# Optimization experiments

Hardware: AMD Instinct MI355X
Metric: run time of the kernel (lower is better)

## Reference

```python
import jax, jax.numpy as jnp
import numpy as np

NUM_EMBEDDINGS = 1024
EMBEDDING_DIM = 64
COMMITMENT_COST = 0.25


def setup_inputs() -> dict:
    key = jax.random.key(0)
    k1, k2 = jax.random.split(key)
    z = jax.random.normal(k1, (32, EMBEDDING_DIM, 32, 32), dtype=jnp.float32)
    # matches nn.Embedding init: uniform(-1/K, 1/K)
    codebook = jax.random.uniform(
        k2, (NUM_EMBEDDINGS, EMBEDDING_DIM), dtype=jnp.float32,
        minval=-1.0 / NUM_EMBEDDINGS, maxval=1.0 / NUM_EMBEDDINGS)
    return {"z": z, "codebook": codebook}


def reference(z, codebook):
    B, C, H, W = z.shape  # C == embedding_dim
    zp = jnp.transpose(z, (0, 2, 3, 1))          # [B,H,W,C]
    z_flat = zp.reshape(-1, C)                    # [N,C], N=B*H*W
    # squared euclidean distances to every code: [N,K]
    d = (jnp.sum(z_flat ** 2, axis=1, keepdims=True)
         + jnp.sum(codebook ** 2, axis=1)
         - 2.0 * jnp.matmul(z_flat, codebook.T))
    indices = jnp.argmin(d, axis=1)               # [N]
    z_q = codebook[indices].reshape(zp.shape)     # [B,H,W,C]
    e_latent_loss = jnp.mean((jax.lax.stop_gradient(z_q) - zp) ** 2)
    q_latent_loss = jnp.mean((z_q - jax.lax.stop_gradient(zp)) ** 2)
    loss = q_latent_loss + COMMITMENT_COST * e_latent_loss
    # straight-through estimator
    z_q_st = zp + jax.lax.stop_gradient(z_q - zp)
    z_q_out = jnp.transpose(z_q_st, (0, 3, 1, 2))  # back to NCHW
    return z_q_out, loss, indices
```

## Files before the change

kernel.cpp:

```cpp
#include <hip/hip_runtime.h>
#include <float.h>


#define DIM       64
#define N_EMB     1024
#define N_PX      32768
#define LOSS_OFF  2097152
#define IDX_OFF   2097153
#define LOSS_SCALE 5.9604644775390625e-07f

__device__ __forceinline__ float np_sumsq64(const float* a) {
    #pragma clang fp contract(off)
    float r[8];
    #pragma unroll
    for (int j = 0; j < 8; ++j) {
        float s = a[j] * a[j];
        #pragma unroll
        for (int m = 1; m < 8; ++m) {
            float p = a[j + 8 * m] * a[j + 8 * m];
            s = s + p;
        }
        r[j] = s;
    }
    return ((r[0] + r[1]) + (r[2] + r[3])) + ((r[4] + r[5]) + (r[6] + r[7]));
}

__global__ __launch_bounds__(256, 4)
void vq_argmin(const float* __restrict__ z, const float* __restrict__ cb,
               float* __restrict__ ws_val, int* __restrict__ ws_idx,
               float* __restrict__ out) {
    __shared__ float esq[256];
    __shared__ float cand_val[4 * 64];
    __shared__ int   cand_idx[4 * 64];

    const int tid  = threadIdx.x;
    const int lane = tid & 63;
    const int wave = __builtin_amdgcn_readfirstlane(tid >> 6);
    const int g    = blockIdx.x >> 2;
    const int s    = blockIdx.x & 3;
    const int n0   = g * 64;
    const int b    = n0 >> 10;
    const int hw0  = n0 & 1023;
    const size_t zbase = (size_t)b * 65536 + (size_t)hw0;

    {
        #pragma clang fp contract(off)
        const int k = s * 256 + tid;
        const float* row = cb + (size_t)k * DIM;
        float r[8];
        #pragma unroll
        for (int j = 0; j < 8; ++j) {
            float acc = row[j] * row[j];
            #pragma unroll
            for (int m = 1; m < 8; ++m) {
                float p = row[j + 8 * m] * row[j + 8 * m];
                acc = acc + p;
            }
            r[j] = acc;
        }
        esq[tid] = ((r[0] + r[1]) + (r[2] + r[3])) + ((r[4] + r[5]) + (r[6] + r[7]));
    }

    float vz[DIM];
    #pragma unroll
    for (int c = 0; c < DIM; ++c)
        vz[c] = z[zbase + (size_t)c * 1024 + lane];
    const float zz = np_sumsq64(vz);

    __syncthreads();

    float best = FLT_MAX;
    int   bidx = 0;
    const int kb = s * 256 + wave * 64;
    for (int kk = 0; kk < 64; kk += 4) {
        const int k = kb + kk;
        const float* e = cb + (size_t)k * DIM;
        float d0 = 0.f, d1 = 0.f, d2 = 0.f, d3 = 0.f;
        #pragma unroll
        for (int c = 0; c < DIM; ++c) {
            const float v = vz[c];
            d0 = __builtin_fmaf(e[c],       v, d0);
            d1 = __builtin_fmaf(e[64 + c],  v, d1);
            d2 = __builtin_fmaf(e[128 + c], v, d2);
            d3 = __builtin_fmaf(e[192 + c], v, d3);
        }
        const int le = wave * 64 + kk;
        float s0, s1, s2, s3;
        {
            #pragma clang fp contract(off)
            const float p0 = zz + esq[le];
            const float p1 = zz + esq[le + 1];
            const float p2 = zz + esq[le + 2];
            const float p3 = zz + esq[le + 3];
            s0 = p0 - 2.0f * d0;
            s1 = p1 - 2.0f * d1;
            s2 = p2 - 2.0f * d2;
            s3 = p3 - 2.0f * d3;
        }
        if (s0 < best) { best = s0; bidx = k; }
        if (s1 < best) { best = s1; bidx = k + 1; }
        if (s2 < best) { best = s2; bidx = k + 2; }
        if (s3 < best) { best = s3; bidx = k + 3; }
    }
    cand_val[wave * 64 + lane] = best;
    cand_idx[wave * 64 + lane] = bidx;
    __syncthreads();

    if (tid < 64) {
        float bv = cand_val[tid];
        int   bi = cand_idx[tid];
        #pragma unroll
        for (int w = 1; w < 4; ++w) {
            float v = cand_val[w * 64 + tid];
            int   i = cand_idx[w * 64 + tid];
            if (v < bv || (v == bv && i < bi)) { bv = v; bi = i; }
        }
        ws_val[s * N_PX + n0 + tid] = bv;
        ws_idx[s * N_PX + n0 + tid] = bi;
    }
    if (blockIdx.x == 0 && tid == 0) out[LOSS_OFF] = 0.f;
}

__global__ __launch_bounds__(256, 4)
void vq_out(const float* __restrict__ z, const float* __restrict__ cb,
            const float* __restrict__ ws_val, const int* __restrict__ ws_idx,
            float* __restrict__ out) {
    __shared__ int   fidx[64];
    __shared__ float lred[4];

    const int tid  = threadIdx.x;
    const int lane = tid & 63;
    const int wave = tid >> 6;
    const int n0   = blockIdx.x * 64;
    const int b    = n0 >> 10;
    const int hw0  = n0 & 1023;
    const size_t zbase = (size_t)b * 65536 + (size_t)hw0;

    if (tid < 64) {
        float bv = ws_val[n0 + tid];
        int   bi = ws_idx[n0 + tid];
        #pragma unroll
        for (int sl = 1; sl < 4; ++sl) {
            float v = ws_val[sl * N_PX + n0 + tid];
            int   i = ws_idx[sl * N_PX + n0 + tid];
            if (v < bv || (v == bv && i < bi)) { bv = v; bi = i; }
        }
        fidx[tid] = bi;
        out[IDX_OFF + n0 + tid] = (float)bi;
    }
    __syncthreads();

    const int px = tid & 63;
    const int cg = tid >> 6;
    const int mi = fidx[px];
    float lacc = 0.f;
    #pragma unroll
    for (int i = 0; i < 16; ++i) {
        const int c = cg * 16 + i;
        float q  = cb[mi * DIM + c];
        size_t go = zbase + (size_t)c * 1024 + px;
        float zv = z[go];
        float d  = q - zv;
        lacc = __builtin_fmaf(d, d, lacc);
        out[go] = q;
    }
    #pragma unroll
    for (int off = 32; off > 0; off >>= 1)
        lacc += __shfl_down(lacc, off, 64);
    if (lane == 0) lred[wave] = lacc;
    __syncthreads();
    if (tid == 0) {
        float t = (lred[0] + lred[1]) + (lred[2] + lred[3]);
        atomicAdd(&out[LOSS_OFF], t * LOSS_SCALE);
    }
}

extern "C" void kernel_launch(void* const* d_in, const int* in_sizes, int n_in,
                              void* d_out, int out_size, void* d_ws, size_t ws_size,
                              hipStream_t stream) {
    const float* z  = (const float*)d_in[0];
    const float* cb = (const float*)d_in[1];
    float* out = (float*)d_out;
    float* ws_val = (float*)d_ws;
    int*   ws_idx = (int*)((char*)d_ws + 4u * N_PX * sizeof(float));

    vq_argmin<<<2048, 256, 0, stream>>>(z, cb, ws_val, ws_idx, out);
    vq_out<<<512, 256, 0, stream>>>(z, cb, ws_val, ws_idx, out);
}
```

Before: 151.5 us.

## Stage z tile in LDS as float4 and unroll codebook loop by eight

Instead of each thread holding 64 z values in registers, the block stages its 64-pixel z tile in shared memory as float4 and reads it back inside the distance loop. This frees VGPRs, and launch bounds are raised to allow 8 blocks per CU for higher occupancy. The codebook loop now handles 8 codes per iteration to reuse each LDS z read across more FMAs. The trade is extra LDS traffic and latency inside the hot loop in exchange for occupancy and fewer global z loads.

```diff
diff --git a/kernel.cpp b/kernel.cpp
--- a/kernel.cpp
+++ b/kernel.cpp
@@ -9,15 +9,15 @@
 #define IDX_OFF   2097153
 #define LOSS_SCALE 5.9604644775390625e-07f
 
-__device__ __forceinline__ float np_sumsq64(const float* a) {
+__device__ __forceinline__ float np_sumsq64_row(const float* __restrict__ row) {
     #pragma clang fp contract(off)
     float r[8];
     #pragma unroll
     for (int j = 0; j < 8; ++j) {
-        float s = a[j] * a[j];
+        float s = row[j] * row[j];
         #pragma unroll
         for (int m = 1; m < 8; ++m) {
-            float p = a[j + 8 * m] * a[j + 8 * m];
+            float p = row[j + 8 * m] * row[j + 8 * m];
             s = s + p;
         }
         r[j] = s;
@@ -25,13 +25,14 @@
     return ((r[0] + r[1]) + (r[2] + r[3])) + ((r[4] + r[5]) + (r[6] + r[7]));
 }
 
-__global__ __launch_bounds__(256, 4)
+__global__ __launch_bounds__(256, 8)
 void vq_argmin(const float* __restrict__ z, const float* __restrict__ cb,
                float* __restrict__ ws_val, int* __restrict__ ws_idx,
                float* __restrict__ out) {
-    __shared__ float esq[256];
-    __shared__ float cand_val[4 * 64];
-    __shared__ int   cand_idx[4 * 64];
+    __shared__ float4 ldsZ[16 * 64];
+    __shared__ float  esq[256];
+    __shared__ float  cand_val[4 * 64];
+    __shared__ int    cand_idx[4 * 64];
 
     const int tid  = threadIdx.x;
     const int lane = tid & 63;
@@ -44,63 +45,83 @@
     const size_t zbase = (size_t)b * 65536 + (size_t)hw0;
 
     {
+        const int px = tid & 63;
+        const int cq = tid >> 6;
+        #pragma unroll
+        for (int r = 0; r < 4; ++r) {
+            const int c4 = cq * 4 + r;
+            const float* zp = z + zbase + (size_t)(c4 * 4) * 1024 + px;
+            float4 v;
+            v.x = zp[0];
+            v.y = zp[1024];
+            v.z = zp[2048];
+            v.w = zp[3072];
+            ldsZ[c4 * 64 + px] = v;
+        }
+    }
+
+    esq[tid] = np_sumsq64_row(cb + (size_t)(s * 256 + tid) * DIM);
+
+    __syncthreads();
+
+    float zz;
+    {
         #pragma clang fp contract(off)
-        const int k = s * 256 + tid;
-        const float* row = cb + (size_t)k * DIM;
-        float r[8];
-        #pragma unroll
-        for (int j = 0; j < 8; ++j) {
-            float acc = row[j] * row[j];
-            #pragma unroll
-            for (int m = 1; m < 8; ++m) {
-                float p = row[j + 8 * m] * row[j + 8 * m];
-                acc = acc + p;
-            }
-            r[j] = acc;
-        }
-        esq[tid] = ((r[0] + r[1]) + (r[2] + r[3])) + ((r[4] + r[5]) + (r[6] + r[7]));
-    }
-
-    float vz[DIM];
-    #pragma unroll
-    for (int c = 0; c < DIM; ++c)
-        vz[c] = z[zbase + (size_t)c * 1024 + lane];
-    const float zz = np_sumsq64(vz);
-
-    __syncthreads();
+        float4 qa = ldsZ[lane];
+        float4 qb = ldsZ[64 + lane];
+        float r0 = qa.x * qa.x, r1 = qa.y * qa.y, r2 = qa.z * qa.z, r3 = qa.w * qa.w;
+        float r4 = qb.x * qb.x, r5 = qb.y * qb.y, r6 = qb.z * qb.z, r7 = qb.w * qb.w;
+        #pragma unroll
+        for (int m = 1; m < 8; ++m) {
+            qa = ldsZ[(2 * m) * 64 + lane];
+            qb = ldsZ[(2 * m + 1) * 64 + lane];
+            float p;
+            p = qa.x * qa.x; r0 = r0 + p;
+            p = qa.y * qa.y; r1 = r1 + p;
+            p = qa.z * qa.z; r2 = r2 + p;
+            p = qa.w * qa.w; r3 = r3 + p;
+            p = qb.x * qb.x; r4 = r4 + p;
+            p = qb.y * qb.y; r5 = r5 + p;
+            p = qb.z * qb.z; r6 = r6 + p;
+            p = qb.w * qb.w; r7 = r7 + p;
+        }
+        zz = ((r0 + r1) + (r2 + r3)) + ((r4 + r5) + (r6 + r7));
+    }
 
     float best = FLT_MAX;
     int   bidx = 0;
     const int kb = s * 256 + wave * 64;
-    for (int kk = 0; kk < 64; kk += 4) {
-        const int k = kb + kk;
-        const float* e = cb + (size_t)k * DIM;
+    const int lb = wave * 64;
+    for (int kk = 0; kk < 64; kk += 8) {
+        const float* e = cb + (size_t)(kb + kk) * DIM;
         float d0 = 0.f, d1 = 0.f, d2 = 0.f, d3 = 0.f;
-        #pragma unroll
-        for (int c = 0; c < DIM; ++c) {
-            const float v = vz[c];
-            d0 = __builtin_fmaf(e[c],       v, d0);
-            d1 = __builtin_fmaf(e[64 + c],  v, d1);
-            d2 = __builtin_fmaf(e[128 + c], v, d2);
-            d3 = __builtin_fmaf(e[192 + c], v, d3);
-        }
-        const int le = wave * 64 + kk;
-        float s0, s1, s2, s3;
-        {
-            #pragma clang fp contract(off)
-            const float p0 = zz + esq[le];
-            const float p1 = zz + esq[le + 1];
-            const float p2 = zz + esq[le + 2];
-            const float p3 = zz + esq[le + 3];
-            s0 = p0 - 2.0f * d0;
-            s1 = p1 - 2.0f * d1;
-            s2 = p2 - 2.0f * d2;
-            s3 = p3 - 2.0f * d3;
-        }
-        if (s0 < best) { best = s0; bidx = k; }
-        if (s1 < best) { best = s1; bidx = k + 1; }
-        if (s2 < best) { best = s2; bidx = k + 2; }
-        if (s3 < best) { best = s3; bidx = k + 3; }
+        float d4 = 0.f, d5 = 0.f, d6 = 0.f, d7 = 0.f;
+        #pragma unroll
+        for (int c4 = 0; c4 < 16; ++c4) {
+            const float4 vzc = ldsZ[c4 * 64 + lane];
+            const int c0 = c4 * 4;
+#define VQ_FMA4(DJ, J) \
+            DJ = __builtin_fmaf(e[(J)*DIM + c0    ], vzc.x, DJ); \
+            DJ = __builtin_fmaf(e[(J)*DIM + c0 + 1], vzc.y, DJ); \
+            DJ = __builtin_fmaf(e[(J)*DIM + c0 + 2], vzc.z, DJ); \
+            DJ = __builtin_fmaf(e[(J)*DIM + c0 + 3], vzc.w, DJ);
+            VQ_FMA4(d0, 0) VQ_FMA4(d1, 1) VQ_FMA4(d2, 2) VQ_FMA4(d3, 3)
+            VQ_FMA4(d4, 4) VQ_FMA4(d5, 5) VQ_FMA4(d6, 6) VQ_FMA4(d7, 7)
+#undef VQ_FMA4
+        }
+#define VQ_SCORE(DJ, J) \
+        { \
+            float sc; \
+            { \
+                _Pragma("clang fp contract(off)") \
+                const float p = zz + esq[lb + kk + (J)]; \
+                sc = p - 2.0f * DJ; \
+            } \
+            if (sc < best) { best = sc; bidx = kb + kk + (J); } \
+        }
+        VQ_SCORE(d0, 0) VQ_SCORE(d1, 1) VQ_SCORE(d2, 2) VQ_SCORE(d3, 3)
+        VQ_SCORE(d4, 4) VQ_SCORE(d5, 5) VQ_SCORE(d6, 6) VQ_SCORE(d7, 7)
+#undef VQ_SCORE
     }
     cand_val[wave * 64 + lane] = best;
     cand_idx[wave * 64 + lane] = bidx;
```

Measured after the change: 297.4 us. +96.3%, slower.
